# Performance work log

Hardware: AMD Instinct MI355X
Metric: run time of the kernel (lower is better)

Reference implementation:

```python
import jax, jax.numpy as jnp
import numpy as np

N, C, H, K = 100000, 64, 8, 16
D = C // H  # head_dim = 8


def setup_inputs() -> dict:
    key = jax.random.key(0)
    ks = jax.random.split(key, 7)
    s = 1.0 / np.sqrt(C)
    return {
        "feats": jax.random.normal(ks[0], (N, C), jnp.float32),
        "knn_idx": jax.random.randint(ks[1], (N, K), 0, N, jnp.int32),
        "Wq": jax.random.normal(ks[2], (C, C), jnp.float32) * s,
        "Wk": jax.random.normal(ks[3], (C, C), jnp.float32) * s,
        "Wv": jax.random.normal(ks[4], (C, C), jnp.float32) * s,
        "Wo": jax.random.normal(ks[5], (C, C), jnp.float32) * s,
        "bo": jnp.zeros((C,), jnp.float32),
    }


def reference(feats, knn_idx, Wq, Wk, Wv, Wo, bo):
    # Projections (torch Linear y = x @ W^T expressed with pre-transposed W)
    q = (feats @ Wq).reshape(N, H, D)          # [N,H,D]
    k_feat = (feats @ Wk).reshape(N, H, D)     # [N,H,D]
    v = (feats @ Wv).reshape(N, H, D)          # [N,H,D]

    # Gather k-NN neighbors: [N,K,H,D]
    k_nb = k_feat[knn_idx]
    v_nb = v[knn_idx]

    # Scores: dot(q, k_neighbor) per head, scaled
    scores = jnp.einsum("nhd,nkhd->nkh", q, k_nb) / np.sqrt(D).astype(np.float32)
    attn = jax.nn.softmax(scores, axis=1)      # softmax over K neighbors

    out = jnp.einsum("nkh,nkhd->nhd", attn, v_nb).reshape(N, C)
    return out @ Wo + bo
```

## Files before the change

kernel.cpp:

```cpp
#include <hip/hip_runtime.h>
#include <hip/hip_fp16.h>
#include <math.h>

#define NPTS 100000
#define CDIM 64
#define KNN  16

typedef unsigned int uint;
typedef _Float16 f16x8 __attribute__((ext_vector_type(8)));
typedef float    f32x4 __attribute__((ext_vector_type(4)));

template <int CTRL>
__device__ __forceinline__ __half dpp_add_h(__half x) {
    int xi = (int)__half_as_ushort(x);
    int yi = __builtin_amdgcn_mov_dpp(xi, CTRL, 0xF, 0xF, true);
    return __hadd(x, __ushort_as_half((unsigned short)yi));
}

__device__ __forceinline__ uint pkrtz(float a, float b) {
    union { __fp16 __attribute__((ext_vector_type(2))) h; uint u; } cv;
    cv.h = __builtin_amdgcn_cvt_pkrtz(a, b);
    return cv.u;
}


__global__ __launch_bounds__(256) void pack_w(
    const float* __restrict__ Wq, const float* __restrict__ Wk,
    const float* __restrict__ Wv, const float* __restrict__ Wo,
    __half* __restrict__ frag)
{
    const float* Ws[4] = {Wq, Wk, Wv, Wo};
    const float scale[4] = {0.3535533905932738f * 1.4426950408889634f, 1.f, 1.f, 1.f};
    f16x8* fp = (f16x8*)frag;
    const int e = blockIdx.x * 256 + threadIdx.x;
    const int lane = e & 63;
    const int ks   = (e >> 6) & 1;
    const int ct   = (e >> 7) & 3;
    const int mat  = e >> 9;
    const int m = lane & 15, quad = lane >> 4;
    const float* W = Ws[mat];
    const float sc = scale[mat];
    f16x8 b;
    #pragma unroll
    for (int j = 0; j < 8; ++j)
        b[j] = (_Float16)(sc * W[(size_t)(ks * 32 + quad * 8 + j) * 64 + ct * 16 + m]);
    fp[e] = b;
}

__device__ __forceinline__ f16x8 load_bfeat(const float* fp, int ks, int quad) {
    const float4 x0 = *(const float4*)(fp + ks * 32 + quad * 8);
    const float4 x1 = *(const float4*)(fp + ks * 32 + quad * 8 + 4);
    f16x8 a;
    a[0] = (_Float16)x0.x; a[1] = (_Float16)x0.y;
    a[2] = (_Float16)x0.z; a[3] = (_Float16)x0.w;
    a[4] = (_Float16)x1.x; a[5] = (_Float16)x1.y;
    a[6] = (_Float16)x1.z; a[7] = (_Float16)x1.w;
    return a;
}

__global__ __launch_bounds__(256) void proj_qkv(
    const float* __restrict__ feats, const __half* __restrict__ frag,
    __half* __restrict__ q, uint* __restrict__ kv)
{
    const int wid = blockIdx.x * 4 + (threadIdx.x >> 6);
    const int lane = threadIdx.x & 63;
    const int m = lane & 15, quad = lane >> 4;

    const f16x8* fp = (const f16x8*)frag;
    f16x8 Wf[3][4][2];
    #pragma unroll
    for (int mat = 0; mat < 3; ++mat)
        #pragma unroll
        for (int ct = 0; ct < 4; ++ct)
            #pragma unroll
            for (int ks = 0; ks < 2; ++ks)
                Wf[mat][ct][ks] = fp[((mat * 4 + ct) * 2 + ks) * 64 + lane];

    #pragma unroll
    for (int tt = 0; tt < 2; ++tt) {
        const int tile = wid * 2 + tt;
        if (tile >= NPTS / 16) break;
        const int r0 = tile * 16;
        const float* ap = feats + (size_t)(r0 + m) * 64;
        const f16x8 Bf0 = load_bfeat(ap, 0, quad);
        const f16x8 Bf1 = load_bfeat(ap, 1, quad);
        const size_t pt = (size_t)(r0 + m);

        #pragma unroll
        for (int ct = 0; ct < 4; ++ct) {
            f32x4 aq = {0.f, 0.f, 0.f, 0.f};
            f32x4 ak = {0.f, 0.f, 0.f, 0.f};
            f32x4 av = {0.f, 0.f, 0.f, 0.f};
            aq = __builtin_amdgcn_mfma_f32_16x16x32_f16(Wf[0][ct][0], Bf0, aq, 0, 0, 0);
            aq = __builtin_amdgcn_mfma_f32_16x16x32_f16(Wf[0][ct][1], Bf1, aq, 0, 0, 0);
            ak = __builtin_amdgcn_mfma_f32_16x16x32_f16(Wf[1][ct][0], Bf0, ak, 0, 0, 0);
            ak = __builtin_amdgcn_mfma_f32_16x16x32_f16(Wf[1][ct][1], Bf1, ak, 0, 0, 0);
            av = __builtin_amdgcn_mfma_f32_16x16x32_f16(Wf[2][ct][0], Bf0, av, 0, 0, 0);
            av = __builtin_amdgcn_mfma_f32_16x16x32_f16(Wf[2][ct][1], Bf1, av, 0, 0, 0);

            const int ch = ct * 16 + quad * 4;
            uint2 qp;
            qp.x = pkrtz(aq[0], aq[1]);
            qp.y = pkrtz(aq[2], aq[3]);
            *(uint2*)(q + pt * 64 + ch) = qp;
            uint4 kp;
            kp.x = pkrtz(ak[0], av[0]);
            kp.y = pkrtz(ak[1], av[1]);
            kp.z = pkrtz(ak[2], av[2]);
            kp.w = pkrtz(ak[3], av[3]);
            *(uint4*)(kv + pt * 64 + ch) = kp;
        }
    }
}

__global__ __launch_bounds__(256) void attn_out(
    const __half* __restrict__ q, const uint* __restrict__ kv,
    const int* __restrict__ knn, const __half* __restrict__ frag,
    const float* __restrict__ bo, float* __restrict__ out)
{
    __shared__ uint sO[8][36];
    const int t = threadIdx.x;
    const int lane = t & 63;
    const int w = t >> 6;
    const int l32 = lane & 31;
    const int p = lane >> 5;
    const int m = lane & 15, quad = lane >> 4;

    const f16x8* fpb = (const f16x8*)frag;
    const f16x8 Wf0 = fpb[((3 * 4 + w) * 2 + 0) * 64 + lane];
    const f16x8 Wf1 = fpb[((3 * 4 + w) * 2 + 1) * 64 + lane];

    const int n0 = blockIdx.x * 8;
    const int nA = n0 + w * 2;
    const int nB = nA + 1;
    const int n  = nA + p;

    const int* krA = knn + (size_t)nA * KNN;
    const int* krB = knn + (size_t)nB * KNN;
    int idx[KNN];
    #pragma unroll
    for (int i = 0; i < KNN; ++i) idx[i] = p ? krB[i] : krA[i];

    const uint qw = ((const uint*)q)[(size_t)n * 32 + l32];
    const __half2 qh = *(const __half2*)&qw;

    uint2 u[KNN];
    #pragma unroll
    for (int i = 0; i < KNN; ++i)
        u[i] = *(const uint2*)(kv + (size_t)idx[i] * 64 + 2 * l32);

    float sc[KNN];
    __half2 vh[KNN];
    #pragma unroll
    for (int i = 0; i < KNN; ++i) {
        const uint kk = __builtin_amdgcn_perm(u[i].y, u[i].x, 0x05040100u);
        const uint vv = __builtin_amdgcn_perm(u[i].y, u[i].x, 0x07060302u);
        vh[i] = *(const __half2*)&vv;
        const __half2 pr = __hmul2(qh, *(const __half2*)&kk);
        __half s = __hadd(__low2half(pr), __high2half(pr));
        s = dpp_add_h<0xB1>(s);
        s = dpp_add_h<0x4E>(s);
        sc[i] = __builtin_amdgcn_exp2f(__half2float(s));
    }

    float ssum = 0.f;
    #pragma unroll
    for (int i = 0; i < KNN; ++i) ssum += sc[i];
    const float inv = __builtin_amdgcn_rcpf(ssum);

    __half2 acc = __float2half2_rn(0.f);
    #pragma unroll
    for (int i = 0; i < KNN; ++i)
        acc = __hfma2(__float2half2_rn(sc[i]), vh[i], acc);
    acc = __hmul2(acc, __float2half2_rn(inv));

    sO[w * 2 + p][l32] = *(const uint*)&acc;
    __syncthreads();

    const uint4 ow = *(const uint4*)&sO[m & 7][quad * 4];
    const f16x8 Bf = *(const f16x8*)&ow;

    f32x4 ac = {0.f, 0.f, 0.f, 0.f};
    ac = __builtin_amdgcn_mfma_f32_16x16x32_f16(Wf0, Bf, ac, 0, 0, 0);
    const uint4 ow2 = *(const uint4*)&sO[m & 7][16 + quad * 4];
    const f16x8 Bf2 = *(const f16x8*)&ow2;
    ac = __builtin_amdgcn_mfma_f32_16x16x32_f16(Wf1, Bf2, ac, 0, 0, 0);

    if (m < 8) {
        const int ch = w * 16 + quad * 4;
        const float4 bias = *(const float4*)(bo + ch);
        float4 o;
        o.x = ac[0] + bias.x; o.y = ac[1] + bias.y;
        o.z = ac[2] + bias.z; o.w = ac[3] + bias.w;
        *(float4*)(out + (size_t)(n0 + m) * 64 + ch) = o;
    }
}

extern "C" void kernel_launch(void* const* d_in, const int* in_sizes, int n_in,
                              void* d_out, int out_size, void* d_ws, size_t ws_size,
                              hipStream_t stream) {
    const float* feats = (const float*)d_in[0];
    const int*   knn   = (const int*)d_in[1];
    const float* Wq    = (const float*)d_in[2];
    const float* Wk    = (const float*)d_in[3];
    const float* Wv    = (const float*)d_in[4];
    const float* Wo    = (const float*)d_in[5];
    const float* bo    = (const float*)d_in[6];
    float* out = (float*)d_out;

    __half* frag = (__half*)d_ws;
    __half* q_h  = (__half*)((char*)d_ws + 32768);
    uint*   kvb  = (uint*)((char*)d_ws + 32768 +
                           (size_t)NPTS * CDIM * sizeof(__half));

    pack_w<<<8, 256, 0, stream>>>(Wq, Wk, Wv, Wo, frag);
    proj_qkv<<<782, 256, 0, stream>>>(feats, frag, q_h, kvb);
    attn_out<<<NPTS / 8, 256, 0, stream>>>(q_h, kvb, knn, frag, bo, out);
}
```

Baseline: 153.8 us.

## Process four points per wave in attention with fp32 dot2 scores and streaming

Restructures attn_out so each wavefront handles four points (16 lanes per point, 4 channels per lane) instead of two. Neighbor k/v gathers become 16-byte loads, and scores use fp32 fdot2 with one DPP step instead of half-precision adds. Softmax is fused into an online accumulation over two batches of eight neighbors. All 16 MFMA rows now carry real points, so output projection rows are no longer wasted. Nontemporal loads and stores are added for streaming data. The tradeoff is more registers per lane and fewer lanes per point.

```diff
diff --git a/kernel.cpp b/kernel.cpp
--- a/kernel.cpp
+++ b/kernel.cpp
@@ -8,13 +8,27 @@
 
 typedef unsigned int uint;
 typedef _Float16 f16x8 __attribute__((ext_vector_type(8)));
+typedef _Float16 f16x2 __attribute__((ext_vector_type(2)));
 typedef float    f32x4 __attribute__((ext_vector_type(4)));
+typedef int      i32x4 __attribute__((ext_vector_type(4)));
+typedef uint     u32x4 __attribute__((ext_vector_type(4)));
+typedef uint     u32x2 __attribute__((ext_vector_type(2)));
 
 template <int CTRL>
-__device__ __forceinline__ __half dpp_add_h(__half x) {
-    int xi = (int)__half_as_ushort(x);
-    int yi = __builtin_amdgcn_mov_dpp(xi, CTRL, 0xF, 0xF, true);
-    return __hadd(x, __ushort_as_half((unsigned short)yi));
+__device__ __forceinline__ float dpp_add_f(float x) {
+    int yi = __builtin_amdgcn_mov_dpp(__float_as_int(x), CTRL, 0xF, 0xF, true);
+    return x + __int_as_float(yi);
+}
+
+__device__ __forceinline__ float dot2acc(uint a, uint b, float c) {
+#if __has_builtin(__builtin_amdgcn_fdot2)
+    return __builtin_amdgcn_fdot2(__builtin_bit_cast(f16x2, a),
+                                  __builtin_bit_cast(f16x2, b), c, false);
+#else
+    const f16x2 ha = __builtin_bit_cast(f16x2, a);
+    const f16x2 hb = __builtin_bit_cast(f16x2, b);
+    return c + (float)ha[0] * (float)hb[0] + (float)ha[1] * (float)hb[1];
+#endif
 }
 
 __device__ __forceinline__ uint pkrtz(float a, float b) {
@@ -48,13 +62,13 @@
 }
 
 __device__ __forceinline__ f16x8 load_bfeat(const float* fp, int ks, int quad) {
-    const float4 x0 = *(const float4*)(fp + ks * 32 + quad * 8);
-    const float4 x1 = *(const float4*)(fp + ks * 32 + quad * 8 + 4);
+    const f32x4 x0 = __builtin_nontemporal_load((const f32x4*)(fp + ks * 32 + quad * 8));
+    const f32x4 x1 = __builtin_nontemporal_load((const f32x4*)(fp + ks * 32 + quad * 8 + 4));
     f16x8 a;
-    a[0] = (_Float16)x0.x; a[1] = (_Float16)x0.y;
-    a[2] = (_Float16)x0.z; a[3] = (_Float16)x0.w;
-    a[4] = (_Float16)x1.x; a[5] = (_Float16)x1.y;
-    a[6] = (_Float16)x1.z; a[7] = (_Float16)x1.w;
+    a[0] = (_Float16)x0[0]; a[1] = (_Float16)x0[1];
+    a[2] = (_Float16)x0[2]; a[3] = (_Float16)x0[3];
+    a[4] = (_Float16)x1[0]; a[5] = (_Float16)x1[1];
+    a[6] = (_Float16)x1[2]; a[7] = (_Float16)x1[3];
     return a;
 }
 
@@ -118,82 +132,79 @@
     const int* __restrict__ knn, const __half* __restrict__ frag,
     const float* __restrict__ bo, float* __restrict__ out)
 {
-    __shared__ uint sO[8][36];
+    __shared__ uint sO[16][36];
     const int t = threadIdx.x;
     const int lane = t & 63;
     const int w = t >> 6;
-    const int l32 = lane & 31;
-    const int p = lane >> 5;
+    const int l16 = lane & 15;
+    const int p4 = lane >> 4;
     const int m = lane & 15, quad = lane >> 4;
+
+    const int n0 = blockIdx.x * 16;
+    const int n  = n0 + w * 4 + p4;
+
+    const i32x4* kp = (const i32x4*)knn + (size_t)n * 4;
+    const i32x4 i0 = __builtin_nontemporal_load(kp);
+    const i32x4 i1 = __builtin_nontemporal_load(kp + 1);
+    const i32x4 i2 = __builtin_nontemporal_load(kp + 2);
+    const i32x4 i3 = __builtin_nontemporal_load(kp + 3);
+    const int idx[KNN] = {i0[0], i0[1], i0[2], i0[3], i1[0], i1[1], i1[2], i1[3],
+                          i2[0], i2[1], i2[2], i2[3], i3[0], i3[1], i3[2], i3[3]};
+
+    const u32x2 qw = __builtin_nontemporal_load((const u32x2*)q + (size_t)n * 16 + l16);
+
+    float ssum = 0.f;
+    __half2 acc01 = __float2half2_rn(0.f);
+    __half2 acc23 = __float2half2_rn(0.f);
+
+    #pragma unroll
+    for (int bb = 0; bb < 2; ++bb) {
+        u32x4 u[8];
+        #pragma unroll
+        for (int i = 0; i < 8; ++i)
+            u[i] = *(const u32x4*)(kv + (size_t)idx[bb * 8 + i] * 64 + 4 * l16);
+        #pragma unroll
+        for (int i = 0; i < 8; ++i) {
+            const uint kk01 = __builtin_amdgcn_perm(u[i][1], u[i][0], 0x05040100u);
+            const uint kk23 = __builtin_amdgcn_perm(u[i][3], u[i][2], 0x05040100u);
+            const uint vv01 = __builtin_amdgcn_perm(u[i][1], u[i][0], 0x07060302u);
+            const uint vv23 = __builtin_amdgcn_perm(u[i][3], u[i][2], 0x07060302u);
+            float s = dot2acc(qw[1], kk23, dot2acc(qw[0], kk01, 0.f));
+            s = dpp_add_f<0xB1>(s);
+            const float e = __builtin_amdgcn_exp2f(s);
+            ssum += e;
+            const __half2 w2 = __float2half2_rn(e);
+            acc01 = __hfma2(w2, *(const __half2*)&vv01, acc01);
+            acc23 = __hfma2(w2, *(const __half2*)&vv23, acc23);
+        }
+    }
+
+    const float inv = __builtin_amdgcn_rcpf(ssum);
+    const __half2 iv = __float2half2_rn(inv);
+    acc01 = __hmul2(acc01, iv);
+    acc23 = __hmul2(acc23, iv);
+    u32x2 ov;
+    ov[0] = *(const uint*)&acc01;
+    ov[1] = *(const uint*)&acc23;
+    *(u32x2*)&sO[w * 4 + p4][2 * l16] = ov;
+    __syncthreads();
 
     const f16x8* fpb = (const f16x8*)frag;
     const f16x8 Wf0 = fpb[((3 * 4 + w) * 2 + 0) * 64 + lane];
     const f16x8 Wf1 = fpb[((3 * 4 + w) * 2 + 1) * 64 + lane];
 
-    const int n0 = blockIdx.x * 8;
-    const int nA = n0 + w * 2;
-    const int nB = nA + 1;
-    const int n  = nA + p;
-
-    const int* krA = knn + (size_t)nA * KNN;
-    const int* krB = knn + (size_t)nB * KNN;
-    int idx[KNN];
-    #pragma unroll
-    for (int i = 0; i < KNN; ++i) idx[i] = p ? krB[i] : krA[i];
-
-    const uint qw = ((const uint*)q)[(size_t)n * 32 + l32];
-    const __half2 qh = *(const __half2*)&qw;
-
-    uint2 u[KNN];
-    #pragma unroll
-    for (int i = 0; i < KNN; ++i)
-        u[i] = *(const uint2*)(kv + (size_t)idx[i] * 64 + 2 * l32);
-
-    float sc[KNN];
-    __half2 vh[KNN];
-    #pragma unroll
-    for (int i = 0; i < KNN; ++i) {
-        const uint kk = __builtin_amdgcn_perm(u[i].y, u[i].x, 0x05040100u);
-        const uint vv = __builtin_amdgcn_perm(u[i].y, u[i].x, 0x07060302u);
-        vh[i] = *(const __half2*)&vv;
-        const __half2 pr = __hmul2(qh, *(const __half2*)&kk);
-        __half s = __hadd(__low2half(pr), __high2half(pr));
-        s = dpp_add_h<0xB1>(s);
-        s = dpp_add_h<0x4E>(s);
-        sc[i] = __builtin_amdgcn_exp2f(__half2float(s));
-    }
-
-    float ssum = 0.f;
-    #pragma unroll
-    for (int i = 0; i < KNN; ++i) ssum += sc[i];
-    const float inv = __builtin_amdgcn_rcpf(ssum);
-
-    __half2 acc = __float2half2_rn(0.f);
-    #pragma unroll
-    for (int i = 0; i < KNN; ++i)
-        acc = __hfma2(__float2half2_rn(sc[i]), vh[i], acc);
-    acc = __hmul2(acc, __float2half2_rn(inv));
-
-    sO[w * 2 + p][l32] = *(const uint*)&acc;
-    __syncthreads();
-
-    const uint4 ow = *(const uint4*)&sO[m & 7][quad * 4];
-    const f16x8 Bf = *(const f16x8*)&ow;
-
+    const f16x8 Bf  = *(const f16x8*)&sO[m][quad * 4];
+    const f16x8 Bf2 = *(const f16x8*)&sO[m][16 + quad * 4];
     f32x4 ac = {0.f, 0.f, 0.f, 0.f};
     ac = __builtin_amdgcn_mfma_f32_16x16x32_f16(Wf0, Bf, ac, 0, 0, 0);
-    const uint4 ow2 = *(const uint4*)&sO[m & 7][16 + quad * 4];
-    const f16x8 Bf2 = *(const f16x8*)&ow2;
     ac = __builtin_amdgcn_mfma_f32_16x16x32_f16(Wf1, Bf2, ac, 0, 0, 0);
 
-    if (m < 8) {
-        const int ch = w * 16 + quad * 4;
-        const float4 bias = *(const float4*)(bo + ch);
-        float4 o;
-        o.x = ac[0] + bias.x; o.y = ac[1] + bias.y;
-        o.z = ac[2] + bias.z; o.w = ac[3] + bias.w;
-        *(float4*)(out + (size_t)(n0 + m) * 64 + ch) = o;
-    }
+    const int ch = w * 16 + quad * 4;
+    const f32x4 bias = *(const f32x4*)(bo + ch);
+    f32x4 o;
+    o[0] = ac[0] + bias[0]; o[1] = ac[1] + bias[1];
+    o[2] = ac[2] + bias[2]; o[3] = ac[3] + bias[3];
+    __builtin_nontemporal_store(o, (f32x4*)(out + (size_t)(n0 + m) * 64 + ch));
 }
 
 extern "C" void kernel_launch(void* const* d_in, const int* in_sizes, int n_in,
@@ -215,5 +226,5 @@
 
     pack_w<<<8, 256, 0, stream>>>(Wq, Wk, Wv, Wo, frag);
     proj_qkv<<<782, 256, 0, stream>>>(feats, frag, q_h, kvb);
-    attn_out<<<NPTS / 8, 256, 0, stream>>>(q_h, kvb, knn, frag, bo, out);
-}
+    attn_out<<<NPTS / 16, 256, 0, stream>>>(q_h, kvb, knn, frag, bo, out);
+}
```

After: 157.8 us. 2.6% more time.
